# Kernel tuning notes

Hardware: AMD Instinct MI355X
Metric: run time of the kernel (lower is better)

Reference implementation:

```python
import jax, jax.numpy as jnp
import numpy as np

BITS = 4
GROUP = 128
IN_F = 4096
OUT_F = 11008
N_GROUPS = IN_F // GROUP  # padded_in == in_features here


def fwht(v):
    """Orthonormal fast Walsh-Hadamard transform over the last axis (len = power of 2)."""
    orig = v.shape
    g = orig[-1]
    x = v.reshape(-1, g)
    h = 1
    while h < g:
        x = x.reshape(-1, g // (2 * h), 2, h)
        a, b = x[:, :, 0, :], x[:, :, 1, :]
        x = jnp.stack([a + b, a - b], axis=2).reshape(-1, g)
        h *= 2
    return (x * (1.0 / np.sqrt(g))).reshape(orig)


def setup_inputs() -> dict:
    key = jax.random.key(0)
    ks = jax.random.split(key, 7)
    x = jax.random.normal(ks[0], (4096, IN_F), dtype=jnp.float32)
    # packed 4-bit indices: two per byte, stored as int32 byte values
    packed_weight = jax.random.randint(ks[1], (OUT_F, IN_F // 2), 0, 256, dtype=jnp.int32)
    # per-(row, group) scale factors (positive)
    norms = jax.random.uniform(ks[2], (OUT_F, N_GROUPS), dtype=jnp.float32) * 0.1 + 0.01
    # Lloyd-Max codebook: 2^bits sorted centroids
    centroids = jnp.sort(jax.random.normal(ks[3], (2 ** BITS,), dtype=jnp.float32))
    # Rademacher sign vectors for the two-round signed WHT rotation
    signs1 = jnp.where(jax.random.normal(ks[4], (GROUP,)) >= 0, 1.0, -1.0).astype(jnp.float32)
    signs2 = jnp.where(jax.random.normal(ks[5], (GROUP,)) >= 0, 1.0, -1.0).astype(jnp.float32)
    bias = jax.random.normal(ks[6], (OUT_F,), dtype=jnp.float32) * 0.01
    return {"x": x, "packed_weight": packed_weight, "norms": norms,
            "centroids": centroids, "signs1": signs1, "signs2": signs2, "bias": bias}


def dequantize(packed_weight, norms, centroids, signs1, signs2):
    out_f, n_groups = norms.shape
    # unpack 4-bit nibbles: low nibble at even positions, high nibble at odd
    pw = packed_weight.astype(jnp.uint8)
    lo = (pw & 15).astype(jnp.int32)
    hi = (pw >> 4).astype(jnp.int32)
    idx = jnp.stack([lo, hi], axis=-1).reshape(out_f, -1)      # [out, padded_in]
    c = centroids[idx].reshape(out_f, n_groups, GROUP)          # codebook lookup
    # inverse of rotate(v) = H(s2 * H(s1 * v)):  v = s1 * H(s2 * H(u))
    u = fwht(c) * signs2
    u = fwht(u) * signs1
    w = u * norms[:, :, None]                                   # per-group rescale
    return w.reshape(out_f, -1)


def reference(x, packed_weight, norms, centroids, signs1, signs2, bias):
    w = dequantize(packed_weight, norms, centroids, signs1, signs2)[:, : x.shape[-1]]
    return x @ w.T + bias
```

## Files before the change

### kernel.cpp

```cpp
#include <hip/hip_runtime.h>
#include <stdint.h>

#define M_DIM 4096
#define K_DIM 4096
#define N_DIM 11008
#define N_GROUPS 32

typedef __attribute__((ext_vector_type(8))) short short8;
typedef __attribute__((ext_vector_type(4))) float floatx4;

__device__ __forceinline__ unsigned short f32_to_bf16(float f) {
    unsigned int u = __float_as_uint(f);
    unsigned int rounding = 0x7FFFu + ((u >> 16) & 1u);
    return (unsigned short)((u + rounding) >> 16);
}

__global__ __launch_bounds__(128) void make_M_kernel(
    const float* __restrict__ signs1, const float* __restrict__ signs2,
    unsigned short* __restrict__ Mt)
{
    const int i = blockIdx.x;
    const int j = threadIdx.x;
    __shared__ float s2s[128];
    s2s[j] = signs2[j];
    __syncthreads();
    float acc = 0.f;
#pragma unroll 8
    for (int a = 0; a < 128; ++a) {
        int par = (__popc(i & a) + __popc(a & j)) & 1;
        acc += par ? -s2s[a] : s2s[a];
    }
    Mt[i * 128 + j] = f32_to_bf16(signs1[j] * acc * (1.0f / 128.0f));
}

#define TX_RS 136

__global__ __launch_bounds__(256) void transform_x_kernel(
    const float* __restrict__ x,
    const unsigned short* __restrict__ Mt,
    unsigned short* __restrict__ z)
{
    __shared__ __align__(16) short Xs[64 * TX_RS];
    __shared__ __align__(16) short Ms[128 * TX_RS];

    const int tid = threadIdx.x;
    const int wave = tid >> 6, lane = tid & 63;
    const int col16 = lane & 15, quad = lane >> 4;
    const int m0 = (blockIdx.x >> 5) * 64;
    const int g = blockIdx.x & 31;
    const int c0 = g * 128;

#pragma unroll
    for (int it = 0; it < 8; ++it) {
        int idx = tid + 256 * it;
        int row = idx >> 5, c4 = idx & 31;
        float4 v = *(const float4*)(x + (size_t)(m0 + row) * K_DIM + c0 + c4 * 4);
        uint2 o;
        o.x = (unsigned)f32_to_bf16(v.x) | ((unsigned)f32_to_bf16(v.y) << 16);
        o.y = (unsigned)f32_to_bf16(v.z) | ((unsigned)f32_to_bf16(v.w) << 16);
        *(uint2*)(Xs + row * TX_RS + c4 * 4) = o;
    }
#pragma unroll
    for (int it = 0; it < 8; ++it) {
        int ch = tid + 256 * it;
        int row = ch >> 4, cc = ch & 15;
        uint4 v = *(const uint4*)(Mt + (size_t)ch * 8);
        *(uint4*)(Ms + row * TX_RS + cc * 8) = v;
    }
    __syncthreads();

    floatx4 acc[8] = {};
#pragma unroll
    for (int ks = 0; ks < 4; ++ks) {
        short8 af = *(const short8*)(Xs + (wave * 16 + col16) * TX_RS + ks * 32 + quad * 8);
#pragma unroll
        for (int ni = 0; ni < 8; ++ni) {
            short8 bf = *(const short8*)(Ms + (ni * 16 + col16) * TX_RS + ks * 32 + quad * 8);
            acc[ni] = __builtin_amdgcn_mfma_f32_16x16x32_bf16(af, bf, acc[ni], 0, 0, 0);
        }
    }
#pragma unroll
    for (int ni = 0; ni < 8; ++ni)
#pragma unroll
        for (int r = 0; r < 4; ++r) {
            int row = m0 + wave * 16 + quad * 4 + r;
            z[(size_t)row * K_DIM + c0 + ni * 16 + col16] = f32_to_bf16(acc[ni][r]);
        }
}

__global__ __launch_bounds__(256) void dequant_lut_kernel(
    const int* __restrict__ packed,
    const float* __restrict__ norms,
    const float* __restrict__ centroids,
    unsigned int* __restrict__ w_out)
{
    __shared__ float2 lut[256];
    const int tid = threadIdx.x;
    lut[tid] = make_float2(centroids[tid & 15], centroids[tid >> 4]);
    __syncthreads();

    const int row = blockIdx.x;
    const int g = tid >> 3;
    const float nrm = norms[row * N_GROUPS + g];
    const int* prow = packed + (size_t)row * 2048 + tid * 8;
    int4 pa = *(const int4*)(prow);
    int4 pb = *(const int4*)(prow + 4);
    int v[8] = {pa.x, pa.y, pa.z, pa.w, pb.x, pb.y, pb.z, pb.w};
    unsigned o[8];
#pragma unroll
    for (int q = 0; q < 8; ++q) {
        float2 c = lut[v[q] & 255];
        o[q] = (unsigned)f32_to_bf16(c.x * nrm) | ((unsigned)f32_to_bf16(c.y * nrm) << 16);
    }
    unsigned* orow = w_out + (size_t)row * 2048 + tid * 8;
    *(uint4*)(orow)     = make_uint4(o[0], o[1], o[2], o[3]);
    *(uint4*)(orow + 4) = make_uint4(o[4], o[5], o[6], o[7]);
}

#define BM 256
#define BN 256
#define BK 64

typedef const __attribute__((address_space(1))) void* gvp_t;
typedef __attribute__((address_space(3))) void* svp_t;

#define BARRIER() do { asm volatile("" ::: "memory"); __builtin_amdgcn_s_barrier(); \
                       asm volatile("" ::: "memory"); } while (0)
#define VM8()   asm volatile("s_waitcnt vmcnt(8)" ::: "memory")
#define VM4()   asm volatile("s_waitcnt vmcnt(4)" ::: "memory")
#define VM2()   asm volatile("s_waitcnt vmcnt(2)" ::: "memory")
#define VM0()   asm volatile("s_waitcnt vmcnt(0)" ::: "memory")
#define PRIO1() __builtin_amdgcn_s_setprio(1)
#define PRIO0() __builtin_amdgcn_s_setprio(0)

__device__ __forceinline__ void read_a4(short8 (&dst)[4][2], const short* rb, int s0) {
#pragma unroll
    for (int fm = 0; fm < 4; ++fm) {
        dst[fm][0] = *(const short8*)(rb + fm * 1024 + s0);
        dst[fm][1] = *(const short8*)(rb + fm * 1024 + (s0 ^ 32));
    }
}
__device__ __forceinline__ void read_b2(short8 (&dst)[2][2], const short* rb, int s0) {
#pragma unroll
    for (int fn = 0; fn < 2; ++fn) {
        dst[fn][0] = *(const short8*)(rb + fn * 1024 + s0);
        dst[fn][1] = *(const short8*)(rb + fn * 1024 + (s0 ^ 32));
    }
}
__device__ __forceinline__ void mfma_q(floatx4 (&acc)[4][2],
                                       const short8 (&a)[4][2], const short8 (&b)[2][2]) {
#pragma unroll
    for (int ks = 0; ks < 2; ++ks)
#pragma unroll
        for (int fm = 0; fm < 4; ++fm)
#pragma unroll
            for (int fn = 0; fn < 2; ++fn)
                acc[fm][fn] = __builtin_amdgcn_mfma_f32_16x16x32_bf16(
                    a[fm][ks], b[fn][ks], acc[fm][fn], 0, 0, 0);
}

__global__ __launch_bounds__(512, 2) void gemm_bt_kernel(
    const unsigned short* __restrict__ A,
    const unsigned short* __restrict__ B,
    const float* __restrict__ bias,
    float* __restrict__ C)
{
    __shared__ __align__(16) short smem[65536];
    short* As = smem;
    short* Bs = smem + 32768;

    const int tid = threadIdx.x;
    const int w = tid >> 6, lane = tid & 63;
    const int wm = w >> 2, wn = w & 3;
    const int col16 = lane & 15, quad = lane >> 4;

    const int bid = blockIdx.x;
    const int mt = bid & 15;
    const int nt = bid >> 4;
    const int m0 = mt * BM, n0 = nt * BN;

    const int gc = (lane & 7) ^ (lane >> 3);
    const unsigned short* aSrc = A + (size_t)(m0 + w * 8 + (lane >> 3)) * K_DIM + gc * 8;
    const unsigned short* bSrc = B + (size_t)(n0 + (w >> 2) * 64 + (w & 3) * 8 + (lane >> 3)) * K_DIM + gc * 8;
    const int wOff = w * 512;

#define STAGE_A(BUF, H, KT) do { \
    __builtin_amdgcn_global_load_lds((gvp_t)(aSrc + (size_t)((H) * 64) * K_DIM + (KT) * 64), \
        (svp_t)(As + (BUF) * 16384 + (H) * 8192 + wOff), 16, 0, 0); \
    __builtin_amdgcn_global_load_lds((gvp_t)(aSrc + (size_t)((H) * 64 + 128) * K_DIM + (KT) * 64), \
        (svp_t)(As + (BUF) * 16384 + (H) * 8192 + 4096 + wOff), 16, 0, 0); \
} while (0)
#define STAGE_B(BUF, H, KT) do { \
    __builtin_amdgcn_global_load_lds((gvp_t)(bSrc + (size_t)((H) * 32) * K_DIM + (KT) * 64), \
        (svp_t)(Bs + (BUF) * 16384 + (H) * 8192 + wOff), 16, 0, 0); \
    __builtin_amdgcn_global_load_lds((gvp_t)(bSrc + (size_t)((H) * 32 + 128) * K_DIM + (KT) * 64), \
        (svp_t)(Bs + (BUF) * 16384 + (H) * 8192 + 4096 + wOff), 16, 0, 0); \
} while (0)

    const short* aR = As + (wm * 64 + col16) * 64;
    const short* bR = Bs + (wn * 32 + col16) * 64;
    const int s0 = (quad ^ (col16 & 7)) << 3;

    short8 a0[4][2], a1[4][2], b0[2][2], b1[2][2];
    floatx4 acc[2][2][4][2];
#pragma unroll
    for (int i0 = 0; i0 < 2; ++i0)
#pragma unroll
        for (int i1 = 0; i1 < 2; ++i1)
#pragma unroll
            for (int i2 = 0; i2 < 4; ++i2)
#pragma unroll
                for (int i3 = 0; i3 < 2; ++i3)
                    acc[i0][i1][i2][i3] = (floatx4)0.0f;


    STAGE_A(0, 0, 0); STAGE_B(0, 0, 0);
    STAGE_A(0, 1, 0); STAGE_B(0, 1, 0);
    STAGE_A(1, 0, 1); STAGE_B(1, 0, 1);
    VM8();
    BARRIER();
    read_a4(a0, aR, s0); read_b2(b0, bR, s0);
    STAGE_A(1, 1, 1);
    VM8();
    BARRIER();

    const int NIT = K_DIM / (2 * BK) - 1;
    for (int i = 0; i < NIT; ++i) {
        const int t = 2 * i;
        read_a4(a1, aR + 8192, s0);
        PRIO1(); mfma_q(acc[0][0], a0, b0); PRIO0();
        STAGE_B(1, 1, t + 1);
        VM8(); BARRIER();
        read_b2(b1, bR + 8192, s0);
        PRIO1(); mfma_q(acc[1][0], a1, b0); PRIO0();
        STAGE_A(0, 0, t + 2);
        BARRIER();
        PRIO1(); mfma_q(acc[0][1], a0, b1); PRIO0();
        STAGE_B(0, 0, t + 2);
        VM8(); BARRIER();
        read_a4(a0, aR + 16384, s0); read_b2(b0, bR + 16384, s0);
        PRIO1(); mfma_q(acc[1][1], a1, b1); PRIO0();
        STAGE_A(0, 1, t + 2);
        VM8(); BARRIER();
        read_a4(a1, aR + 16384 + 8192, s0);
        PRIO1(); mfma_q(acc[0][0], a0, b0); PRIO0();
        STAGE_B(0, 1, t + 2);
        VM8(); BARRIER();
        read_b2(b1, bR + 16384 + 8192, s0);
        PRIO1(); mfma_q(acc[1][0], a1, b0); PRIO0();
        STAGE_A(1, 0, t + 3);
        BARRIER();
        PRIO1(); mfma_q(acc[0][1], a0, b1); PRIO0();
        STAGE_B(1, 0, t + 3);
        VM8(); BARRIER();
        read_a4(a0, aR, s0); read_b2(b0, bR, s0);
        PRIO1(); mfma_q(acc[1][1], a1, b1); PRIO0();
        STAGE_A(1, 1, t + 3);
        VM8(); BARRIER();
    }

    read_a4(a1, aR + 8192, s0);
    mfma_q(acc[0][0], a0, b0);
    STAGE_B(1, 1, 63);
    VM8();
    BARRIER();
    read_b2(b1, bR + 8192, s0);
    mfma_q(acc[1][0], a1, b0);
    VM4();
    BARRIER();
    mfma_q(acc[0][1], a0, b1);
    VM2();
    BARRIER();
    read_a4(a0, aR + 16384, s0); read_b2(b0, bR + 16384, s0);
    mfma_q(acc[1][1], a1, b1);
    VM0();
    BARRIER();
    read_a4(a1, aR + 16384 + 8192, s0);
    mfma_q(acc[0][0], a0, b0);
    read_b2(b1, bR + 16384 + 8192, s0);
    mfma_q(acc[1][0], a1, b0);
    mfma_q(acc[0][1], a0, b1);
    mfma_q(acc[1][1], a1, b1);

#undef STAGE_A
#undef STAGE_B

    float bv[2][2];
#pragma unroll
    for (int qn = 0; qn < 2; ++qn)
#pragma unroll
        for (int fn = 0; fn < 2; ++fn)
            bv[qn][fn] = bias[n0 + wn * 64 + qn * 32 + fn * 16 + col16];

#pragma unroll
    for (int qm = 0; qm < 2; ++qm)
#pragma unroll
        for (int fm = 0; fm < 4; ++fm)
#pragma unroll
            for (int r = 0; r < 4; ++r) {
                float* crow = C + (size_t)(m0 + wm * 128 + qm * 64 + fm * 16 + quad * 4 + r) * N_DIM
                              + n0 + wn * 64 + col16;
#pragma unroll
                for (int qn = 0; qn < 2; ++qn)
#pragma unroll
                    for (int fn = 0; fn < 2; ++fn)
                        crow[qn * 32 + fn * 16] = acc[qm][qn][fm][fn][r] + bv[qn][fn];
            }
}

extern "C" void kernel_launch(void* const* d_in, const int* in_sizes, int n_in,
                              void* d_out, int out_size, void* d_ws, size_t ws_size,
                              hipStream_t stream) {
    const float* x        = (const float*)d_in[0];
    const int* packed     = (const int*)d_in[1];
    const float* norms    = (const float*)d_in[2];
    const float* centroids= (const float*)d_in[3];
    const float* signs1   = (const float*)d_in[4];
    const float* signs2   = (const float*)d_in[5];
    const float* bias     = (const float*)d_in[6];
    float* out            = (float*)d_out;

    unsigned short* Mt     = (unsigned short*)d_ws;
    unsigned short* w_bf16 = (unsigned short*)((char*)d_ws + 32768);
    unsigned short* z_bf16 = (unsigned short*)((char*)d_ws + 32768 + (size_t)N_DIM * K_DIM * 2);

    make_M_kernel<<<128, 128, 0, stream>>>(signs1, signs2, Mt);

    transform_x_kernel<<<(M_DIM / 64) * N_GROUPS, 256, 0, stream>>>(x, Mt, z_bf16);

    dequant_lut_kernel<<<N_DIM, 256, 0, stream>>>(
        packed, norms, centroids, (unsigned int*)w_bf16);

    gemm_bt_kernel<<<dim3((M_DIM / BM) * (N_DIM / BN)), 512, 0, stream>>>(
        z_bf16, w_bf16, bias, out);
}
```

Measured before the change: 593.8 us.

## Switch GEMM to 32x32x16 MFMA and restructure x-transform with staged output

The main GEMM now uses 32x32x16 bf16 MFMA instructions instead of 16x16x32. This means fewer MFMA issues and fewer LDS fragment reads per tile, and it changes both the fragment read pattern and the epilogue layout. The x-transform kernel now uses 512 threads that each handle 256 rows per block. It loads the rotation matrix fragments into registers once and loops over four 64-row slabs. Results are staged through LDS so z is written with coalesced 16-byte stores. The risks are higher accumulator register pressure and the correctness of the new swizzled read addressing.

```diff
diff --git a/kernel.cpp b/kernel.cpp
--- a/kernel.cpp
+++ b/kernel.cpp
@@ -8,6 +8,7 @@
 
 typedef __attribute__((ext_vector_type(8))) short short8;
 typedef __attribute__((ext_vector_type(4))) float floatx4;
+typedef __attribute__((ext_vector_type(16))) float floatx16;
 
 __device__ __forceinline__ unsigned short f32_to_bf16(float f) {
     unsigned int u = __float_as_uint(f);
@@ -33,59 +34,88 @@
     Mt[i * 128 + j] = f32_to_bf16(signs1[j] * acc * (1.0f / 128.0f));
 }
 
-#define TX_RS 136
-
-__global__ __launch_bounds__(256) void transform_x_kernel(
+__global__ __launch_bounds__(512) void transform_x_kernel(
     const float* __restrict__ x,
     const unsigned short* __restrict__ Mt,
     unsigned short* __restrict__ z)
 {
-    __shared__ __align__(16) short Xs[64 * TX_RS];
-    __shared__ __align__(16) short Ms[128 * TX_RS];
+    __shared__ __align__(16) short Ms[128 * 136];
+    __shared__ __align__(16) short Xs[64 * 136];
+    __shared__ __align__(16) short Ls[64 * 136];
 
     const int tid = threadIdx.x;
     const int wave = tid >> 6, lane = tid & 63;
     const int col16 = lane & 15, quad = lane >> 4;
-    const int m0 = (blockIdx.x >> 5) * 64;
+    const int wr = wave >> 2;
+    const int wc = wave & 3;
     const int g = blockIdx.x & 31;
+    const int mblk = blockIdx.x >> 5;
     const int c0 = g * 128;
-
-#pragma unroll
-    for (int it = 0; it < 8; ++it) {
-        int idx = tid + 256 * it;
-        int row = idx >> 5, c4 = idx & 31;
-        float4 v = *(const float4*)(x + (size_t)(m0 + row) * K_DIM + c0 + c4 * 4);
-        uint2 o;
-        o.x = (unsigned)f32_to_bf16(v.x) | ((unsigned)f32_to_bf16(v.y) << 16);
-        o.y = (unsigned)f32_to_bf16(v.z) | ((unsigned)f32_to_bf16(v.w) << 16);
-        *(uint2*)(Xs + row * TX_RS + c4 * 4) = o;
-    }
-#pragma unroll
-    for (int it = 0; it < 8; ++it) {
-        int ch = tid + 256 * it;
+    const int mBase = mblk * 256;
+
+#pragma unroll
+    for (int it = 0; it < 4; ++it) {
+        int ch = tid + 512 * it;
         int row = ch >> 4, cc = ch & 15;
-        uint4 v = *(const uint4*)(Mt + (size_t)ch * 8);
-        *(uint4*)(Ms + row * TX_RS + cc * 8) = v;
+        *(uint4*)(Ms + row * 136 + cc * 8) = *(const uint4*)(Mt + (size_t)ch * 8);
     }
     __syncthreads();
 
-    floatx4 acc[8] = {};
-#pragma unroll
-    for (int ks = 0; ks < 4; ++ks) {
-        short8 af = *(const short8*)(Xs + (wave * 16 + col16) * TX_RS + ks * 32 + quad * 8);
-#pragma unroll
-        for (int ni = 0; ni < 8; ++ni) {
-            short8 bf = *(const short8*)(Ms + (ni * 16 + col16) * TX_RS + ks * 32 + quad * 8);
-            acc[ni] = __builtin_amdgcn_mfma_f32_16x16x32_bf16(af, bf, acc[ni], 0, 0, 0);
+    short8 bf[2][4];
+#pragma unroll
+    for (int ni = 0; ni < 2; ++ni)
+#pragma unroll
+        for (int ks = 0; ks < 4; ++ks)
+            bf[ni][ks] = *(const short8*)(Ms + (wc * 32 + ni * 16 + col16) * 136 + ks * 32 + quad * 8);
+
+    for (int s = 0; s < 4; ++s) {
+        __syncthreads();
+#pragma unroll
+        for (int it = 0; it < 4; ++it) {
+            int idx = tid + 512 * it;
+            int row = idx >> 5, c4 = idx & 31;
+            float4 v = *(const float4*)(x + (size_t)(mBase + s * 64 + row) * K_DIM + c0 + c4 * 4);
+            uint2 o;
+            o.x = (unsigned)f32_to_bf16(v.x) | ((unsigned)f32_to_bf16(v.y) << 16);
+            o.y = (unsigned)f32_to_bf16(v.z) | ((unsigned)f32_to_bf16(v.w) << 16);
+            *(uint2*)(Xs + row * 136 + c4 * 4) = o;
         }
-    }
-#pragma unroll
-    for (int ni = 0; ni < 8; ++ni)
-#pragma unroll
-        for (int r = 0; r < 4; ++r) {
-            int row = m0 + wave * 16 + quad * 4 + r;
-            z[(size_t)row * K_DIM + c0 + ni * 16 + col16] = f32_to_bf16(acc[ni][r]);
+        __syncthreads();
+
+        short8 af[2][4];
+#pragma unroll
+        for (int mi = 0; mi < 2; ++mi)
+#pragma unroll
+            for (int ks = 0; ks < 4; ++ks)
+                af[mi][ks] = *(const short8*)(Xs + (wr * 32 + mi * 16 + col16) * 136 + ks * 32 + quad * 8);
+        floatx4 acc2[2][2] = {};
+#pragma unroll
+        for (int ks = 0; ks < 4; ++ks)
+#pragma unroll
+            for (int mi = 0; mi < 2; ++mi)
+#pragma unroll
+                for (int ni = 0; ni < 2; ++ni)
+                    acc2[mi][ni] = __builtin_amdgcn_mfma_f32_16x16x32_bf16(
+                        af[mi][ks], bf[ni][ks], acc2[mi][ni], 0, 0, 0);
+
+#pragma unroll
+        for (int mi = 0; mi < 2; ++mi)
+#pragma unroll
+            for (int ni = 0; ni < 2; ++ni)
+#pragma unroll
+                for (int r = 0; r < 4; ++r)
+                    Ls[(wr * 32 + mi * 16 + quad * 4 + r) * 136 + wc * 32 + ni * 16 + col16] =
+                        f32_to_bf16(acc2[mi][ni][r]);
+        __syncthreads();
+
+#pragma unroll
+        for (int it = 0; it < 2; ++it) {
+            int idx = tid + 512 * it;
+            int row = idx >> 4, cc = idx & 15;
+            uint4 v = *(const uint4*)(Ls + row * 136 + cc * 8);
+            *(uint4*)(z + (size_t)(mBase + s * 64 + row) * K_DIM + c0 + cc * 8) = v;
         }
+    }
 }
 
 __global__ __launch_bounds__(256) void dequant_lut_kernel(
@@ -133,30 +163,25 @@
 #define PRIO1() __builtin_amdgcn_s_setprio(1)
 #define PRIO0() __builtin_amdgcn_s_setprio(0)
 
-__device__ __forceinline__ void read_a4(short8 (&dst)[4][2], const short* rb, int s0) {
-#pragma unroll
-    for (int fm = 0; fm < 4; ++fm) {
-        dst[fm][0] = *(const short8*)(rb + fm * 1024 + s0);
-        dst[fm][1] = *(const short8*)(rb + fm * 1024 + (s0 ^ 32));
-    }
-}
-__device__ __forceinline__ void read_b2(short8 (&dst)[2][2], const short* rb, int s0) {
-#pragma unroll
-    for (int fn = 0; fn < 2; ++fn) {
-        dst[fn][0] = *(const short8*)(rb + fn * 1024 + s0);
-        dst[fn][1] = *(const short8*)(rb + fn * 1024 + (s0 ^ 32));
-    }
-}
-__device__ __forceinline__ void mfma_q(floatx4 (&acc)[4][2],
-                                       const short8 (&a)[4][2], const short8 (&b)[2][2]) {
-#pragma unroll
-    for (int ks = 0; ks < 2; ++ks)
-#pragma unroll
-        for (int fm = 0; fm < 4; ++fm)
-#pragma unroll
-            for (int fn = 0; fn < 2; ++fn)
-                acc[fm][fn] = __builtin_amdgcn_mfma_f32_16x16x32_bf16(
-                    a[fm][ks], b[fn][ks], acc[fm][fn], 0, 0, 0);
+__device__ __forceinline__ void read_a32(short8 (&dst)[2][4], const short* rb, int hh, int r7) {
+#pragma unroll
+    for (int mi = 0; mi < 2; ++mi)
+#pragma unroll
+        for (int k = 0; k < 4; ++k)
+            dst[mi][k] = *(const short8*)(rb + mi * 2048 + ((((k << 1) | hh) ^ r7) << 3));
+}
+__device__ __forceinline__ void read_b32(short8 (&dst)[4], const short* rb, int hh, int r7) {
+#pragma unroll
+    for (int k = 0; k < 4; ++k)
+        dst[k] = *(const short8*)(rb + ((((k << 1) | hh) ^ r7) << 3));
+}
+__device__ __forceinline__ void mfma_q32(floatx16 (&acc)[2],
+                                         const short8 (&a)[2][4], const short8 (&b)[4]) {
+#pragma unroll
+    for (int k = 0; k < 4; ++k)
+#pragma unroll
+        for (int mi = 0; mi < 2; ++mi)
+            acc[mi] = __builtin_amdgcn_mfma_f32_32x32x16_bf16(a[mi][k], b[k], acc[mi], 0, 0, 0);
 }
 
 __global__ __launch_bounds__(512, 2) void gemm_bt_kernel(
@@ -172,7 +197,7 @@
     const int tid = threadIdx.x;
     const int w = tid >> 6, lane = tid & 63;
     const int wm = w >> 2, wn = w & 3;
-    const int col16 = lane & 15, quad = lane >> 4;
+    const int l31 = lane & 31, hh = lane >> 5, r7 = lane & 7;
 
     const int bid = blockIdx.x;
     const int mt = bid & 15;
@@ -197,21 +222,18 @@
         (svp_t)(Bs + (BUF) * 16384 + (H) * 8192 + 4096 + wOff), 16, 0, 0); \
 } while (0)
 
-    const short* aR = As + (wm * 64 + col16) * 64;
-    const short* bR = Bs + (wn * 32 + col16) * 64;
-    const int s0 = (quad ^ (col16 & 7)) << 3;
-
-    short8 a0[4][2], a1[4][2], b0[2][2], b1[2][2];
-    floatx4 acc[2][2][4][2];
+    const short* aR = As + (wm * 64 + l31) * 64;
+    const short* bR = Bs + (wn * 32 + l31) * 64;
+
+    short8 a0[2][4], a1[2][4], b0[4], b1[4];
+    floatx16 acc[2][2][2];
 #pragma unroll
     for (int i0 = 0; i0 < 2; ++i0)
 #pragma unroll
         for (int i1 = 0; i1 < 2; ++i1)
 #pragma unroll
-            for (int i2 = 0; i2 < 4; ++i2)
-#pragma unroll
-                for (int i3 = 0; i3 < 2; ++i3)
-                    acc[i0][i1][i2][i3] = (floatx4)0.0f;
+            for (int i2 = 0; i2 < 2; ++i2)
+                acc[i0][i1][i2] = (floatx16)0.0f;
 
 
     STAGE_A(0, 0, 0); STAGE_B(0, 0, 0);
@@ -219,7 +241,7 @@
     STAGE_A(1, 0, 1); STAGE_B(1, 0, 1);
     VM8();
     BARRIER();
-    read_a4(a0, aR, s0); read_b2(b0, bR, s0);
+    read_a32(a0, aR, hh, r7); read_b32(b0, bR, hh, r7);
     STAGE_A(1, 1, 1);
     VM8();
     BARRIER();
@@ -227,84 +249,82 @@
     const int NIT = K_DIM / (2 * BK) - 1;
     for (int i = 0; i < NIT; ++i) {
         const int t = 2 * i;
-        read_a4(a1, aR + 8192, s0);
-        PRIO1(); mfma_q(acc[0][0], a0, b0); PRIO0();
+        read_a32(a1, aR + 8192, hh, r7);
+        PRIO1(); mfma_q32(acc[0][0], a0, b0); PRIO0();
         STAGE_B(1, 1, t + 1);
         VM8(); BARRIER();
-        read_b2(b1, bR + 8192, s0);
-        PRIO1(); mfma_q(acc[1][0], a1, b0); PRIO0();
+        read_b32(b1, bR + 8192, hh, r7);
+        PRIO1(); mfma_q32(acc[1][0], a1, b0); PRIO0();
         STAGE_A(0, 0, t + 2);
         BARRIER();
-        PRIO1(); mfma_q(acc[0][1], a0, b1); PRIO0();
+        PRIO1(); mfma_q32(acc[0][1], a0, b1); PRIO0();
         STAGE_B(0, 0, t + 2);
         VM8(); BARRIER();
-        read_a4(a0, aR + 16384, s0); read_b2(b0, bR + 16384, s0);
-        PRIO1(); mfma_q(acc[1][1], a1, b1); PRIO0();
+        read_a32(a0, aR + 16384, hh, r7); read_b32(b0, bR + 16384, hh, r7);
+        PRIO1(); mfma_q32(acc[1][1], a1, b1); PRIO0();
         STAGE_A(0, 1, t + 2);
         VM8(); BARRIER();
-        read_a4(a1, aR + 16384 + 8192, s0);
-        PRIO1(); mfma_q(acc[0][0], a0, b0); PRIO0();
+        read_a32(a1, aR + 16384 + 8192, hh, r7);
+        PRIO1(); mfma_q32(acc[0][0], a0, b0); PRIO0();
         STAGE_B(0, 1, t + 2);
         VM8(); BARRIER();
-        read_b2(b1, bR + 16384 + 8192, s0);
-        PRIO1(); mfma_q(acc[1][0], a1, b0); PRIO0();
+        read_b32(b1, bR + 16384 + 8192, hh, r7);
+        PRIO1(); mfma_q32(acc[1][0], a1, b0); PRIO0();
         STAGE_A(1, 0, t + 3);
         BARRIER();
-        PRIO1(); mfma_q(acc[0][1], a0, b1); PRIO0();
+        PRIO1(); mfma_q32(acc[0][1], a0, b1); PRIO0();
         STAGE_B(1, 0, t + 3);
         VM8(); BARRIER();
-        read_a4(a0, aR, s0); read_b2(b0, bR, s0);
-        PRIO1(); mfma_q(acc[1][1], a1, b1); PRIO0();
+        read_a32(a0, aR, hh, r7); read_b32(b0, bR, hh, r7);
+        PRIO1(); mfma_q32(acc[1][1], a1, b1); PRIO0();
         STAGE_A(1, 1, t + 3);
         VM8(); BARRIER();
     }
 
-    read_a4(a1, aR + 8192, s0);
-    mfma_q(acc[0][0], a0, b0);
+    read_a32(a1, aR + 8192, hh, r7);
+    mfma_q32(acc[0][0], a0, b0);
     STAGE_B(1, 1, 63);
     VM8();
     BARRIER();
-    read_b2(b1, bR + 8192, s0);
-    mfma_q(acc[1][0], a1, b0);
+    read_b32(b1, bR + 8192, hh, r7);
+    mfma_q32(acc[1][0], a1, b0);
     VM4();
     BARRIER();
-    mfma_q(acc[0][1], a0, b1);
+    mfma_q32(acc[0][1], a0, b1);
     VM2();
     BARRIER();
-    read_a4(a0, aR + 16384, s0); read_b2(b0, bR + 16384, s0);
-    mfma_q(acc[1][1], a1, b1);
+    read_a32(a0, aR + 16384, hh, r7); read_b32(b0, bR + 16384, hh, r7);
+    mfma_q32(acc[1][1], a1, b1);
     VM0();
     BARRIER();
-    read_a4(a1, aR + 16384 + 8192, s0);
-    mfma_q(acc[0][0], a0, b0);
-    read_b2(b1, bR + 16384 + 8192, s0);
-    mfma_q(acc[1][0], a1, b0);
-    mfma_q(acc[0][1], a0, b1);
-    mfma_q(acc[1][1], a1, b1);
+    read_a32(a1, aR + 16384 + 8192, hh, r7);
+    mfma_q32(acc[0][0], a0, b0);
+    read_b32(b1, bR + 16384 + 8192, hh, r7);
+    mfma_q32(acc[1][0], a1, b0);
+    mfma_q32(acc[0][1], a0, b1);
+    mfma_q32(acc[1][1], a1, b1);
 
 #undef STAGE_A
 #undef STAGE_B
 
-    float bv[2][2];
+    float bvq[2];
 #pragma unroll
     for (int qn = 0; qn < 2; ++qn)
-#pragma unroll
-        for (int fn = 0; fn < 2; ++fn)
-            bv[qn][fn] = bias[n0 + wn * 64 + qn * 32 + fn * 16 + col16];
+        bvq[qn] = bias[n0 + wn * 64 + qn * 32 + l31];
 
 #pragma unroll
     for (int qm = 0; qm < 2; ++qm)
 #pragma unroll
-        for (int fm = 0; fm < 4; ++fm)
-#pragma unroll
-            for (int r = 0; r < 4; ++r) {
-                float* crow = C + (size_t)(m0 + wm * 128 + qm * 64 + fm * 16 + quad * 4 + r) * N_DIM
-                              + n0 + wn * 64 + col16;
-#pragma unroll
-                for (int qn = 0; qn < 2; ++qn)
-#pragma unroll
-                    for (int fn = 0; fn < 2; ++fn)
-                        crow[qn * 32 + fn * 16] = acc[qm][qn][fm][fn][r] + bv[qn][fn];
+        for (int qn = 0; qn < 2; ++qn)
+#pragma unroll
+            for (int mi = 0; mi < 2; ++mi) {
+                const int rbase = m0 + wm * 128 + qm * 64 + mi * 32 + 4 * hh;
+                const long cb = (long)n0 + wn * 64 + qn * 32 + l31;
+#pragma unroll
+                for (int r = 0; r < 16; ++r) {
+                    int row = rbase + (r & 3) + 8 * (r >> 2);
+                    C[(size_t)row * N_DIM + cb] = acc[qm][qn][mi][r] + bvq[qn];
+                }
             }
 }
 
@@ -326,7 +346,7 @@
 
     make_M_kernel<<<128, 128, 0, stream>>>(signs1, signs2, Mt);
 
-    transform_x_kernel<<<(M_DIM / 64) * N_GROUPS, 256, 0, stream>>>(x, Mt, z_bf16);
+    transform_x_kernel<<<(M_DIM / 256) * N_GROUPS, 512, 0, stream>>>(x, Mt, z_bf16);
 
     dequant_lut_kernel<<<N_DIM, 256, 0, stream>>>(
         packed, norms, centroids, (unsigned int*)w_bf16);
```

New measurement: 628.4 us. +5.8%, slower.
